# Optimization experiments

Measured on AMD Instinct MI355X. Metric: run time of the kernel, lower is better.

The kernel has to match this reference:

```python
import jax, jax.numpy as jnp
from jax import lax
import numpy as np

B, C, T = 8, 512, 2048
D = C // 2  # inter_channels
EPS = 1e-5


def setup_inputs() -> dict:
    key = jax.random.key(0)
    ks = jax.random.split(key, 16)
    inp = {}
    inp['x'] = jax.random.normal(ks[0], (B, C, T), dtype=jnp.float32)
    # temporal convs: Conv2d(1, C, kernel=(3, C), dilation=(i+1,1)), no bias, std=0.001
    inp['tc_w1'] = jax.random.normal(ks[1], (C, 1, 3, C), dtype=jnp.float32) * 0.001
    inp['tc_w2'] = jax.random.normal(ks[2], (C, 1, 3, C), dtype=jnp.float32) * 0.001
    # z: Conv1d(3C -> C, k=1)
    inp['z_w'] = jax.random.normal(ks[3], (C, 3 * C), dtype=jnp.float32) * (1.0 / np.sqrt(3 * C))
    inp['z_b'] = jax.random.normal(ks[4], (C,), dtype=jnp.float32) * 0.02
    # g / theta / phi: Conv1d(C -> D, k=1)
    s = 1.0 / np.sqrt(C)
    inp['g_w'] = jax.random.normal(ks[5], (D, C), dtype=jnp.float32) * s
    inp['g_b'] = jax.random.normal(ks[6], (D,), dtype=jnp.float32) * 0.02
    inp['th_w'] = jax.random.normal(ks[7], (D, C), dtype=jnp.float32) * s
    inp['th_b'] = jax.random.normal(ks[8], (D,), dtype=jnp.float32) * 0.02
    inp['ph_w'] = jax.random.normal(ks[9], (D, C), dtype=jnp.float32) * s
    inp['ph_b'] = jax.random.normal(ks[10], (D,), dtype=jnp.float32) * 0.02
    # W: Conv1d(D -> C, k=1) + BatchNorm1d(C) (eval-mode with trained params)
    inp['W_w'] = jax.random.normal(ks[11], (C, D), dtype=jnp.float32) * (1.0 / np.sqrt(D))
    inp['W_b'] = jax.random.normal(ks[12], (C,), dtype=jnp.float32) * 0.02
    inp['bn_g'] = jax.random.normal(ks[13], (C,), dtype=jnp.float32) * 0.1 + 1.0
    inp['bn_b'] = jax.random.normal(ks[14], (C,), dtype=jnp.float32) * 0.1
    inp['bn_mean'] = jax.random.normal(ks[15], (C,), dtype=jnp.float32) * 0.1
    inp['bn_var'] = jax.random.uniform(jax.random.fold_in(key, 99), (C,), dtype=jnp.float32) + 0.5
    return inp


def _pos_encoding(t, c):
    # standard sinusoidal PE, shape (t, c)
    pos = jnp.arange(t, dtype=jnp.float32)[:, None]
    div = jnp.exp(-jnp.log(jnp.float32(10000.0)) * (jnp.arange(0, c, 2, dtype=jnp.float32) / c))
    pe = jnp.zeros((t, c), dtype=jnp.float32)
    pe = pe.at[:, 0::2].set(jnp.sin(pos * div))
    pe = pe.at[:, 1::2].set(jnp.cos(pos * div))
    return pe


def _conv1x1(w, b, x):
    # w: (O, I), x: (b, I, T) -> (b, O, T)
    return jnp.einsum('oi,bit->bot', w, x) + b[None, :, None]


def _tconv(xt, w, d):
    # xt: (b, 1, T, C), w: (C_out, 1, 3, C), dilation d along T, padding (d, 0)
    out = lax.conv_general_dilated(
        xt, w, window_strides=(1, 1), padding=[(d, d), (0, 0)],
        rhs_dilation=(d, 1), dimension_numbers=('NCHW', 'OIHW', 'NCHW'))
    return out[..., 0]  # (b, C_out, T)


def reference(x, tc_w1, tc_w2, z_w, z_b, g_w, g_b, th_w, th_b, ph_w, ph_b,
              W_w, W_b, bn_g, bn_b, bn_mean, bn_var):
    b, c, t = x.shape
    # positional-encoding add: pos (b, T, C) -> permute -> (b, C, T)
    pe = _pos_encoding(t, c)           # (T, C)
    x = x + pe.T[None]                 # (b, C, T)
    # temporal dilated convs over (b, 1, T, C)
    xt = x.transpose(0, 2, 1)[:, None]  # (b, 1, T, C)
    temp = jnp.concatenate([_tconv(xt, tc_w1, 1), _tconv(xt, tc_w2, 2)], axis=1)  # (b, 2C, T)
    xcat = jnp.concatenate([x, temp], axis=1)   # (b, 3C, T)
    x2 = _conv1x1(z_w, z_b, xcat)               # (b, C, T)
    g_x = _conv1x1(g_w, g_b, x2).transpose(0, 2, 1)    # (b, T, D)
    theta_x = _conv1x1(th_w, th_b, x2).transpose(0, 2, 1)  # (b, T, D)
    phi_x = _conv1x1(ph_w, ph_b, x2)            # (b, D, T)
    f = jnp.einsum('btd,bds->bts', theta_x, phi_x)  # unscaled affinity (b, T, T)
    f_div_C = jax.nn.softmax(f, axis=-1)
    y = jnp.einsum('bts,bsd->btd', f_div_C, g_x)    # (b, T, D)
    y = y.transpose(0, 2, 1)                         # (b, D, T)
    wy = _conv1x1(W_w, W_b, y)                       # (b, C, T)
    # BatchNorm1d (eval mode)
    wy = (wy - bn_mean[None, :, None]) * (bn_g / jnp.sqrt(bn_var + EPS))[None, :, None] + bn_b[None, :, None]
    return wy + x2
```

## Files before the change

kernel.cpp:

```cpp
#include <hip/hip_runtime.h>
#include <stdint.h>

typedef _Float16 h8v __attribute__((ext_vector_type(8)));
typedef float f4v __attribute__((ext_vector_type(4)));

#define MFMA(a,b,c) __builtin_amdgcn_mfma_f32_16x16x32_f16((a),(b),(c),0,0,0)
#define NSPLIT 4

__device__ __forceinline__ _Float16 f2h(float f) { return (_Float16)f; }

__device__ __forceinline__ int swb(int row, int chunk) {
  return row * 64 + (((chunk) ^ ((row >> 1) & 3)) << 4);
}

__global__ __launch_bounds__(256) void k_pe_t(const float* __restrict__ x, _Float16* __restrict__ xpe) {
  __shared__ float tile[32][33];
  int b = blockIdx.z;
  int t0 = blockIdx.x * 32, c0 = blockIdx.y * 32;
  int tid = threadIdx.x;
  int col = tid & 31, rowq = tid >> 5;
#pragma unroll
  for (int i = 0; i < 4; ++i) {
    int c = c0 + rowq + i * 8;
    int t = t0 + col;
    int j2 = c & ~1;
    float dv = expf(-0.01798894603885192f * (float)j2);
    float ang = (float)t * dv;
    float pe = (c & 1) ? cosf(ang) : sinf(ang);
    tile[rowq + i * 8][col] = x[((size_t)b * 512 + c) * 2048 + t] + pe;
  }
  __syncthreads();
#pragma unroll
  for (int i = 0; i < 4; ++i) {
    int t = t0 + rowq + i * 8;
    int c = c0 + col;
    xpe[((size_t)b * 2048 + t) * 512 + c] = f2h(tile[col][rowq + i * 8]);
  }
}

__global__ __launch_bounds__(256) void k_cast(const float* __restrict__ a0, const float* __restrict__ a1,
                                              const float* __restrict__ a2, const float* __restrict__ a3,
                                              _Float16* __restrict__ o) {
  int w = blockIdx.y;
  const float* s = (w == 0) ? a0 : (w == 1) ? a1 : (w == 2) ? a2 : a3;
  int i = blockIdx.x * 256 + threadIdx.x;
  o[(size_t)w * 131072 + i] = f2h(s[i]);
}

__global__ __launch_bounds__(256) void k_castz(const float* __restrict__ zw, _Float16* __restrict__ zh) {
  int i = blockIdx.x * 256 + threadIdx.x;
  zh[i] = f2h(zw[i]);
}

__global__ __launch_bounds__(256) void k_wtrans(const float* __restrict__ w1, const float* __restrict__ w2,
                                                _Float16* __restrict__ wt) {
  int z = blockIdx.z;
  const float* src = (z < 3) ? w1 : w2;
  int k = (z < 3) ? z : z - 3;
  __shared__ _Float16 tile[64][65];
  int m0 = blockIdx.y * 64, c0 = blockIdx.x * 64;
  int tid = threadIdx.x;
  int tc = tid & 63, tm = tid >> 6;
#pragma unroll
  for (int i = 0; i < 16; ++i) {
    int m = m0 + tm + i * 4;
    tile[tm + i * 4][tc] = f2h(src[(size_t)m * 1536 + (size_t)k * 512 + c0 + tc]);
  }
  __syncthreads();
#pragma unroll
  for (int i = 0; i < 16; ++i) {
    int c = c0 + tm + i * 4;
    wt[((size_t)z * 512 + c) * 512 + m0 + tc] = tile[tc][tm + i * 4];
  }
}

__global__ __launch_bounds__(256) void k_merge(const _Float16* __restrict__ zh,
                                               const _Float16* __restrict__ wt,
                                               const float* __restrict__ zwf,
                                               _Float16* __restrict__ M) {
  int s = blockIdx.z;
  int wid = threadIdx.x >> 6, lane = threadIdx.x & 63;
  int o0 = blockIdx.y * 64 + (wid >> 1) * 32;
  int c0 = blockIdx.x * 64 + (wid & 1) * 32;
  int row16 = lane & 15, kg = lane >> 4, koff = kg * 8;
  f4v acc[2][2];
#pragma unroll
  for (int mi = 0; mi < 2; ++mi)
#pragma unroll
    for (int ni = 0; ni < 2; ++ni) acc[mi][ni] = (f4v){0.f, 0.f, 0.f, 0.f};

  int np = (s == 2) ? 2 : 1;
  for (int p = 0; p < np; ++p) {
    int seg, wi;
    if (s == 0)      { seg = 1024; wi = 3; }
    else if (s == 1) { seg = 512;  wi = 0; }
    else if (s == 3) { seg = 512;  wi = 2; }
    else if (s == 4) { seg = 1024; wi = 5; }
    else             { seg = (p == 0) ? 512 : 1024; wi = (p == 0) ? 1 : 4; }
    const _Float16* A = zh + seg;
    const _Float16* B = wt + (size_t)wi * 512 * 512;
    for (int k0 = 0; k0 < 512; k0 += 32) {
      h8v a[2], bv[2];
#pragma unroll
      for (int i = 0; i < 2; ++i)
        a[i] = *(const h8v*)(A + (size_t)(o0 + i * 16 + row16) * 1536 + k0 + koff);
#pragma unroll
      for (int i = 0; i < 2; ++i)
        bv[i] = *(const h8v*)(B + (size_t)(c0 + i * 16 + row16) * 512 + k0 + koff);
#pragma unroll
      for (int mi = 0; mi < 2; ++mi)
#pragma unroll
        for (int ni = 0; ni < 2; ++ni)
          acc[mi][ni] = MFMA(a[mi], bv[ni], acc[mi][ni]);
    }
  }
  _Float16* dst = M + (size_t)s * 512 * 512;
#pragma unroll
  for (int mi = 0; mi < 2; ++mi)
#pragma unroll
    for (int r = 0; r < 4; ++r) {
      int o = o0 + mi * 16 + kg * 4 + r;
#pragma unroll
      for (int ni = 0; ni < 2; ++ni) {
        int c = c0 + ni * 16 + row16;
        float v = acc[mi][ni][r];
        if (s == 2) v += zwf[(size_t)o * 1536 + c];
        dst[(size_t)o * 512 + c] = f2h(v);
      }
    }
}

__device__ __forceinline__ void gemm128_lds(const _Float16* __restrict__ L, int ldl,
                                            const _Float16* __restrict__ R, int ldr,
                                            int K, int tid, char* lsA, char* lsB,
                                            f4v acc[4][4]) {
  int wid = tid >> 6, lane = tid & 63;
  int wm = (wid >> 1) * 64, wn = (wid & 1) * 64;
  int row16 = lane & 15, kg = lane >> 4;
  int ar0 = tid >> 2, ar1 = (tid + 256) >> 2, ach = tid & 3;
  h8v pa0, pa1, pb0, pb1;

  pa0 = *(const h8v*)(L + (size_t)ar0 * ldl + ach * 8);
  pa1 = *(const h8v*)(L + (size_t)ar1 * ldl + ach * 8);
  pb0 = *(const h8v*)(R + (size_t)ar0 * ldr + ach * 8);
  pb1 = *(const h8v*)(R + (size_t)ar1 * ldr + ach * 8);
  *(h8v*)(lsA + swb(ar0, ach)) = pa0;
  *(h8v*)(lsA + swb(ar1, ach)) = pa1;
  *(h8v*)(lsB + swb(ar0, ach)) = pb0;
  *(h8v*)(lsB + swb(ar1, ach)) = pb1;
  __syncthreads();

  int nk = K >> 5;
  for (int kc = 0; kc < nk; ++kc) {
    char* ca = lsA + (kc & 1) * 8192;
    char* cb = lsB + (kc & 1) * 8192;
    bool pf = (kc < nk - 1);
    if (pf) {
      int k1 = (kc + 1) << 5;
      pa0 = *(const h8v*)(L + (size_t)ar0 * ldl + k1 + ach * 8);
      pa1 = *(const h8v*)(L + (size_t)ar1 * ldl + k1 + ach * 8);
      pb0 = *(const h8v*)(R + (size_t)ar0 * ldr + k1 + ach * 8);
      pb1 = *(const h8v*)(R + (size_t)ar1 * ldr + k1 + ach * 8);
    }
    h8v a[4], bv[4];
#pragma unroll
    for (int i = 0; i < 4; ++i)
      a[i] = *(const h8v*)(ca + swb(wm + i * 16 + row16, kg));
#pragma unroll
    for (int i = 0; i < 4; ++i)
      bv[i] = *(const h8v*)(cb + swb(wn + i * 16 + row16, kg));
#pragma unroll
    for (int mi = 0; mi < 4; ++mi)
#pragma unroll
      for (int ni = 0; ni < 4; ++ni)
        acc[mi][ni] = MFMA(a[mi], bv[ni], acc[mi][ni]);
    if (pf) {
      char* na = lsA + ((kc & 1) ^ 1) * 8192;
      char* nb = lsB + ((kc & 1) ^ 1) * 8192;
      *(h8v*)(na + swb(ar0, ach)) = pa0;
      *(h8v*)(na + swb(ar1, ach)) = pa1;
      *(h8v*)(nb + swb(ar0, ach)) = pb0;
      *(h8v*)(nb + swb(ar1, ach)) = pb1;
    }
    __syncthreads();
  }
}

__global__ __launch_bounds__(256, 2) void k_conv(const _Float16* __restrict__ Mh,
                                                 const _Float16* __restrict__ xpe,
                                                 const float* __restrict__ zb,
                                                 _Float16* __restrict__ x2ct,
                                                 _Float16* __restrict__ x2h) {
  int b = blockIdx.z;
  int o0 = blockIdx.y * 64, t0 = blockIdx.x * 128;
  int tid = threadIdx.x;
  int wid = tid >> 6, lane = tid & 63;
  int wm = (wid >> 1) * 32, wn = (wid & 1) * 64;
  int row16 = lane & 15, kg = lane >> 4;
  __shared__ __align__(16) char asm2[2][320 * 64];
  __shared__ __align__(16) char bsm[2][132 * 64];
  const _Float16* Xb = xpe + (size_t)b * 2048 * 512;
  const h8v zerov = {0, 0, 0, 0, 0, 0, 0, 0};

  f4v acc[2][4];
#pragma unroll
  for (int mi = 0; mi < 2; ++mi)
#pragma unroll
    for (int ni = 0; ni < 4; ++ni) acc[mi][ni] = (f4v){0.f, 0.f, 0.f, 0.f};

  int arow[5], asrow[5], aorow[5], achk = tid & 3;
#pragma unroll
  for (int j = 0; j < 5; ++j) {
    arow[j] = (tid + 256 * j) >> 2;
    asrow[j] = arow[j] >> 6;
    aorow[j] = arow[j] & 63;
  }
  int br0 = tid >> 2, br1 = (tid + 256) >> 2, br2 = (tid + 512) >> 2;
  int tg0 = t0 + br0 - 2, tg1 = t0 + br1 - 2, tg2 = t0 + br2 - 2;
  bool v0 = (tg0 >= 0 && tg0 < 2048);
  bool v1 = (tg1 >= 0 && tg1 < 2048);
  bool v2 = (tid < 16) && (tg2 >= 0 && tg2 < 2048);
  h8v sa[5], s0, s1, s2;

#pragma unroll
  for (int j = 0; j < 5; ++j)
    sa[j] = *(const h8v*)(Mh + (size_t)asrow[j] * 262144 + (size_t)(o0 + aorow[j]) * 512 + achk * 8);
  s0 = v0 ? *(const h8v*)(Xb + (size_t)tg0 * 512 + achk * 8) : zerov;
  s1 = v1 ? *(const h8v*)(Xb + (size_t)tg1 * 512 + achk * 8) : zerov;
  s2 = v2 ? *(const h8v*)(Xb + (size_t)tg2 * 512 + achk * 8) : zerov;
#pragma unroll
  for (int j = 0; j < 5; ++j) *(h8v*)(&asm2[0][swb(arow[j], achk)]) = sa[j];
  *(h8v*)(&bsm[0][swb(br0, achk)]) = s0;
  *(h8v*)(&bsm[0][swb(br1, achk)]) = s1;
  if (tid < 16) *(h8v*)(&bsm[0][swb(br2, achk)]) = s2;
  __syncthreads();

  for (int kc = 0; kc < 16; ++kc) {
    char* ca = asm2[kc & 1];
    char* cb = bsm[kc & 1];
    bool pf = (kc < 15);
    if (pf) {
      int k1 = (kc + 1) * 32;
#pragma unroll
      for (int j = 0; j < 5; ++j)
        sa[j] = *(const h8v*)(Mh + (size_t)asrow[j] * 262144 + (size_t)(o0 + aorow[j]) * 512 + k1 + achk * 8);
      s0 = v0 ? *(const h8v*)(Xb + (size_t)tg0 * 512 + k1 + achk * 8) : zerov;
      s1 = v1 ? *(const h8v*)(Xb + (size_t)tg1 * 512 + k1 + achk * 8) : zerov;
      s2 = v2 ? *(const h8v*)(Xb + (size_t)tg2 * 512 + k1 + achk * 8) : zerov;
    }
#pragma unroll
    for (int s = 0; s < 5; ++s) {
      h8v a[2];
#pragma unroll
      for (int i = 0; i < 2; ++i)
        a[i] = *(const h8v*)(ca + swb(s * 64 + wm + i * 16 + row16, kg));
#pragma unroll
      for (int ni = 0; ni < 4; ++ni) {
        int rr = wn + ni * 16 + row16 + s;
        h8v bv = *(const h8v*)(cb + swb(rr, kg));
#pragma unroll
        for (int mi = 0; mi < 2; ++mi)
          acc[mi][ni] = MFMA(a[mi], bv, acc[mi][ni]);
      }
    }
    if (pf) {
      char* na = asm2[(kc & 1) ^ 1];
      char* nb = bsm[(kc & 1) ^ 1];
#pragma unroll
      for (int j = 0; j < 5; ++j) *(h8v*)(&na[swb(arow[j], achk)]) = sa[j];
      *(h8v*)(&nb[swb(br0, achk)]) = s0;
      *(h8v*)(&nb[swb(br1, achk)]) = s1;
      if (tid < 16) *(h8v*)(&nb[swb(br2, achk)]) = s2;
    }
    __syncthreads();
  }

#pragma unroll
  for (int mi = 0; mi < 2; ++mi)
#pragma unroll
    for (int r = 0; r < 4; ++r) {
      int o = o0 + wm + mi * 16 + kg * 4 + r;
      float bias = zb[o];
#pragma unroll
      for (int ni = 0; ni < 4; ++ni) {
        int t = t0 + wn + ni * 16 + row16;
        float v = acc[mi][ni][r] + bias;
        x2ct[((size_t)b * 512 + o) * 2048 + t] = f2h(v);
        x2h[((size_t)b * 2048 + t) * 512 + o] = f2h(v);
      }
    }
}

__global__ __launch_bounds__(256, 3) void k_gtp(const _Float16* __restrict__ x2h,
                                                const _Float16* __restrict__ wth, const _Float16* __restrict__ wph,
                                                const _Float16* __restrict__ wg,
                                                const float* __restrict__ thb, const float* __restrict__ phb,
                                                const float* __restrict__ gb,
                                                _Float16* __restrict__ tht, _Float16* __restrict__ pht,
                                                _Float16* __restrict__ gv) {
  int b = blockIdx.z;
  int proj = blockIdx.y >> 1, dtile = blockIdx.y & 1;
  int tid = threadIdx.x;
  int wid = tid >> 6, lane = tid & 63;
  int wm = (wid >> 1) * 64, wn = (wid & 1) * 64;
  int row16 = lane & 15, kg = lane >> 4;
  __shared__ __align__(16) char lA[2][8192];
  __shared__ __align__(16) char lB[2][8192];
  const _Float16* X = x2h + (size_t)b * 2048 * 512;
  f4v acc[4][4];
#pragma unroll
  for (int mi = 0; mi < 4; ++mi)
#pragma unroll
    for (int ni = 0; ni < 4; ++ni) acc[mi][ni] = (f4v){0.f, 0.f, 0.f, 0.f};

  if (proj < 2) {
    const _Float16* W = (proj == 0) ? wth : wph;
    const float* bias = (proj == 0) ? thb : phb;
    _Float16* out = (proj == 0) ? tht : pht;
    int m0 = blockIdx.x * 128, n0 = dtile * 128;
    gemm128_lds(X + (size_t)m0 * 512, 512, W + (size_t)n0 * 512, 512, 512, tid, lA[0], lB[0], acc);
#pragma unroll
    for (int mi = 0; mi < 4; ++mi)
#pragma unroll
      for (int r = 0; r < 4; ++r) {
        int t = m0 + wm + mi * 16 + kg * 4 + r;
#pragma unroll
        for (int ni = 0; ni < 4; ++ni) {
          int d = n0 + wn + ni * 16 + row16;
          out[((size_t)b * 2048 + t) * 256 + d] = f2h(acc[mi][ni][r] + bias[d]);
        }
      }
  } else {
    int m0 = dtile * 128, n0 = blockIdx.x * 128;
    gemm128_lds(wg + (size_t)m0 * 512, 512, X + (size_t)n0 * 512, 512, 512, tid, lA[0], lB[0], acc);
#pragma unroll
    for (int mi = 0; mi < 4; ++mi)
#pragma unroll
      for (int r = 0; r < 4; ++r) {
        int d = m0 + wm + mi * 16 + kg * 4 + r;
        float bias = gb[d];
#pragma unroll
        for (int ni = 0; ni < 4; ++ni) {
          int t = n0 + wn + ni * 16 + row16;
          gv[((size_t)b * 256 + d) * 2048 + t] = f2h(acc[mi][ni][r] + bias);
        }
      }
  }
}

__global__ __launch_bounds__(512) void k_attn(const _Float16* __restrict__ tht,
                                              const _Float16* __restrict__ pht,
                                              const _Float16* __restrict__ gv,
                                              _Float16* __restrict__ yp,
                                              float* __restrict__ mlm, float* __restrict__ mll) {
  int b = blockIdx.z, sp = blockIdx.y;
  int tid = threadIdx.x;
  int wid = tid >> 6, lane = tid & 63;
  int q0 = blockIdx.x * 128 + wid * 16;
  int row16 = lane & 15, kg = lane >> 4, koff = kg * 8;
  int rswz = row16 & 7;

  __shared__ __align__(16) _Float16 kvbuf[32768];
  __shared__ __align__(16) _Float16 p_lds[8][1024];
  char* pw = (char*)&p_lds[wid][0];
  char* cb = (char*)&kvbuf[0];

  const _Float16* thb = tht + (size_t)b * 2048 * 256;
  const _Float16* phb = pht + (size_t)b * 2048 * 256;
  const _Float16* gvb = gv + (size_t)b * 256 * 2048;

  h8v qf[8];
#pragma unroll
  for (int ks = 0; ks < 8; ++ks)
    qf[ks] = *(const h8v*)(thb + (size_t)(q0 + row16) * 256 + ks * 32 + koff);

  float m_i[4], l_i[4];
#pragma unroll
  for (int r = 0; r < 4; ++r) { m_i[r] = -3e38f; l_i[r] = 0.f; }
  f4v yacc[16];
#pragma unroll
  for (int ni = 0; ni < 16; ++ni) yacc[ni] = (f4v){0.f, 0.f, 0.f, 0.f};

  {
    int k0 = sp * 512;
#pragma unroll
    for (int j = 0; j < 4; ++j) {
      int idx = tid + 512 * j;
      h8v kv = *(const h8v*)(phb + (size_t)(k0 + (idx >> 5)) * 256 + (idx & 31) * 8);
      h8v vv = *(const h8v*)(gvb + (size_t)(idx >> 3) * 2048 + k0 + (idx & 7) * 8);
      *(h8v*)(cb + (idx >> 5) * 512 + (((idx & 31) ^ ((idx >> 5) & 7)) << 4)) = kv;
      *(h8v*)(cb + 32768 + (idx >> 3) * 128 + (((idx & 7) ^ ((idx >> 3) & 7)) << 4)) = vv;
    }
  }
  __syncthreads();

  for (int t = 0; t < 8; ++t) {
    int k0 = sp * 512 + t * 64;

    h8v kreg[4], vreg[4];
    bool pf = (t < 7);
    if (pf) {
      int k1 = k0 + 64;
#pragma unroll
      for (int j = 0; j < 4; ++j) {
        int idx = tid + 512 * j;
        kreg[j] = *(const h8v*)(phb + (size_t)(k1 + (idx >> 5)) * 256 + (idx & 31) * 8);
        vreg[j] = *(const h8v*)(gvb + (size_t)(idx >> 3) * 2048 + k1 + (idx & 7) * 8);
      }
    }

    f4v sacc[4];
#pragma unroll
    for (int ni = 0; ni < 4; ++ni) sacc[ni] = (f4v){0.f, 0.f, 0.f, 0.f};
#pragma unroll
    for (int ks = 0; ks < 8; ++ks) {
#pragma unroll
      for (int ni = 0; ni < 4; ++ni) {
        int krow = ni * 16 + row16;
        h8v kf = *(const h8v*)(cb + krow * 512 + ((((ks << 2) | kg) ^ rswz) << 4));
        sacc[ni] = MFMA(qf[ks], kf, sacc[ni]);
      }
    }
    float al[4];
#pragma unroll
    for (int r = 0; r < 4; ++r) {
      float rm = fmaxf(fmaxf(sacc[0][r], sacc[1][r]), fmaxf(sacc[2][r], sacc[3][r]));
#pragma unroll
      for (int m = 1; m <= 8; m <<= 1) rm = fmaxf(rm, __shfl_xor(rm, m, 64));
      float mn = fmaxf(m_i[r], rm);
      al[r] = __expf(m_i[r] - mn);
      m_i[r] = mn;
      float rs = 0.f;
#pragma unroll
      for (int ni = 0; ni < 4; ++ni) {
        float p = __expf(sacc[ni][r] - mn);
        sacc[ni][r] = p;
        rs += p;
      }
#pragma unroll
      for (int m = 1; m <= 8; m <<= 1) rs += __shfl_xor(rs, m, 64);
      l_i[r] = l_i[r] * al[r] + rs;
    }
#pragma unroll
    for (int r = 0; r < 4; ++r) {
      int q = kg * 4 + r;
#pragma unroll
      for (int ni = 0; ni < 4; ++ni) {
        int sx = ni * 16 + row16;
        int byte = (q * 128 + sx * 2) ^ ((q & 7) << 4);
        *(_Float16*)(pw + byte) = f2h(sacc[ni][r]);
      }
    }
#pragma unroll
    for (int ni = 0; ni < 16; ++ni)
#pragma unroll
      for (int r = 0; r < 4; ++r) yacc[ni][r] *= al[r];
#pragma unroll
    for (int ks2 = 0; ks2 < 2; ++ks2) {
      int pbyte = (row16 * 128 + (ks2 * 32 + koff) * 2) ^ (rswz << 4);
      h8v pa = *(const h8v*)(pw + pbyte);
#pragma unroll
      for (int ni = 0; ni < 16; ++ni) {
        int d = ni * 16 + row16;
        h8v vb = *(const h8v*)(cb + 32768 + d * 128 + ((((ks2 << 2) | kg) ^ rswz) << 4));
        yacc[ni] = MFMA(pa, vb, yacc[ni]);
      }
    }
    if (pf) {
      __syncthreads();
#pragma unroll
      for (int j = 0; j < 4; ++j) {
        int idx = tid + 512 * j;
        *(h8v*)(cb + (idx >> 5) * 512 + (((idx & 31) ^ ((idx >> 5) & 7)) << 4)) = kreg[j];
        *(h8v*)(cb + 32768 + (idx >> 3) * 128 + (((idx & 7) ^ ((idx >> 3) & 7)) << 4)) = vreg[j];
      }
      __syncthreads();
    }
  }

  _Float16* yb = yp + (size_t)(sp * 8 + b) * 2048 * 256;
  float* mm = mlm + (size_t)(sp * 8 + b) * 2048;
  float* ml = mll + (size_t)(sp * 8 + b) * 2048;
#pragma unroll
  for (int r = 0; r < 4; ++r) {
    int q = q0 + kg * 4 + r;
#pragma unroll
    for (int ni = 0; ni < 16; ++ni)
      yb[(size_t)q * 256 + ni * 16 + row16] = f2h(yacc[ni][r]);
    if (row16 == 0) { mm[q] = m_i[r]; ml[q] = l_i[r]; }
  }
}

__global__ __launch_bounds__(256) void k_comb(const _Float16* __restrict__ yp,
                                              const float* __restrict__ mlm, const float* __restrict__ mll,
                                              _Float16* __restrict__ yv) {
  int b = blockIdx.y;
  int q = blockIdx.x * 32 + (threadIdx.x >> 3);
  int d0 = (threadIdx.x & 7) * 32;
  float ms[NSPLIT], w[NSPLIT];
  float M = -3e38f;
#pragma unroll
  for (int s = 0; s < NSPLIT; ++s) {
    ms[s] = mlm[(size_t)(s * 8 + b) * 2048 + q];
    M = fmaxf(M, ms[s]);
  }
  float L = 0.f;
#pragma unroll
  for (int s = 0; s < NSPLIT; ++s) {
    w[s] = __expf(ms[s] - M);
    L += w[s] * mll[(size_t)(s * 8 + b) * 2048 + q];
  }
  float inv = 1.f / L;
#pragma unroll
  for (int s = 0; s < NSPLIT; ++s) w[s] *= inv;
  _Float16* out = yv + ((size_t)b * 2048 + q) * 256 + d0;
#pragma unroll
  for (int c = 0; c < 4; ++c) {
    float o[8];
#pragma unroll
    for (int j = 0; j < 8; ++j) o[j] = 0.f;
#pragma unroll
    for (int s = 0; s < NSPLIT; ++s) {
      h8v v = *(const h8v*)(yp + ((size_t)(s * 8 + b) * 2048 + q) * 256 + d0 + c * 8);
#pragma unroll
      for (int j = 0; j < 8; ++j) o[j] += w[s] * (float)v[j];
    }
    h8v ov;
#pragma unroll
    for (int j = 0; j < 8; ++j) ov[j] = f2h(o[j]);
    *(h8v*)(out + c * 8) = ov;
  }
}

__global__ __launch_bounds__(256, 3) void k_final(const _Float16* __restrict__ Wh,
                                                  const _Float16* __restrict__ yv,
                                                  const float* __restrict__ Wb,
                                                  const float* __restrict__ bng, const float* __restrict__ bnb,
                                                  const float* __restrict__ bnm, const float* __restrict__ bnv,
                                                  const _Float16* __restrict__ x2ct, float* __restrict__ out) {
  int b = blockIdx.z;
  int o0 = blockIdx.y * 128, t0 = blockIdx.x * 128;
  int tid = threadIdx.x;
  int wid = tid >> 6, lane = tid & 63;
  int wm = (wid >> 1) * 64, wn = (wid & 1) * 64;
  int row16 = lane & 15, kg = lane >> 4;
  __shared__ __align__(16) char lA[2][8192];
  __shared__ __align__(16) char lB[2][8192];
  f4v acc[4][4];
#pragma unroll
  for (int mi = 0; mi < 4; ++mi)
#pragma unroll
    for (int ni = 0; ni < 4; ++ni) acc[mi][ni] = (f4v){0.f, 0.f, 0.f, 0.f};
  gemm128_lds(Wh + (size_t)o0 * 256, 256,
              yv + (size_t)b * 2048 * 256 + (size_t)t0 * 256, 256, 256, tid, lA[0], lB[0], acc);
#pragma unroll
  for (int mi = 0; mi < 4; ++mi)
#pragma unroll
    for (int r = 0; r < 4; ++r) {
      int o = o0 + wm + mi * 16 + kg * 4 + r;
      float sc = bng[o] * rsqrtf(bnv[o] + 1e-5f);
      float add = (Wb[o] - bnm[o]) * sc + bnb[o];
#pragma unroll
      for (int ni = 0; ni < 4; ++ni) {
        int t = t0 + wn + ni * 16 + row16;
        size_t idx = ((size_t)b * 512 + o) * 2048 + t;
        out[idx] = acc[mi][ni][r] * sc + add + (float)x2ct[idx];
      }
    }
}

extern "C" void kernel_launch(void* const* d_in, const int* in_sizes, int n_in,
                              void* d_out, int out_size, void* d_ws, size_t ws_size,
                              hipStream_t stream) {
  const float* x    = (const float*)d_in[0];
  const float* tcw1 = (const float*)d_in[1];
  const float* tcw2 = (const float*)d_in[2];
  const float* zw   = (const float*)d_in[3];
  const float* zb   = (const float*)d_in[4];
  const float* gw   = (const float*)d_in[5];
  const float* gb   = (const float*)d_in[6];
  const float* thw  = (const float*)d_in[7];
  const float* thb  = (const float*)d_in[8];
  const float* phw  = (const float*)d_in[9];
  const float* phb  = (const float*)d_in[10];
  const float* Ww   = (const float*)d_in[11];
  const float* Wb   = (const float*)d_in[12];
  const float* bng  = (const float*)d_in[13];
  const float* bnb  = (const float*)d_in[14];
  const float* bnm  = (const float*)d_in[15];
  const float* bnv  = (const float*)d_in[16];

  char* Wp = (char*)d_ws;
  _Float16* xpe = (_Float16*)(Wp);
  _Float16* Mh  = (_Float16*)(Wp + 16777216);
  _Float16* x2h = (_Float16*)(Wp + 19398656);
  _Float16* x2c = (_Float16*)(Wp + 36175872);
  _Float16* tht = (_Float16*)(Wp + 69730304);
  _Float16* pht = (_Float16*)(Wp + 78118912);
  _Float16* gv  = (_Float16*)(Wp + 86507520);
  _Float16* yv  = (_Float16*)(Wp + 94896128);
  _Float16* wc  = (_Float16*)(Wp + 103284736);
  _Float16* wth = wc, *wph = wc + 131072, *wg = wc + 262144, *wW = wc + 393216;
  _Float16* zh  = (_Float16*)(Wp + 36175872);
  _Float16* wt  = (_Float16*)(Wp + 36175872 + 1572864);
  _Float16* yp  = (_Float16*)(Wp);
  float*    mlm = (float*)   (Wp + 33554432);
  float*    mll = (float*)   (Wp + 33816576);

  k_cast  <<<dim3(512, 4), 256, 0, stream>>>(thw, phw, gw, Ww, wc);
  k_castz <<<3072, 256, 0, stream>>>(zw, zh);
  k_wtrans<<<dim3(8, 8, 6), 256, 0, stream>>>(tcw1, tcw2, wt);
  k_merge <<<dim3(8, 8, 5), 256, 0, stream>>>(zh, wt, zw, Mh);
  k_pe_t  <<<dim3(64, 16, 8), 256, 0, stream>>>(x, xpe);
  k_conv  <<<dim3(16, 8, 8), 256, 0, stream>>>(Mh, xpe, zb, x2c, x2h);
  k_gtp   <<<dim3(16, 6, 8), 256, 0, stream>>>(x2h, wth, wph, wg, thb, phb, gb, tht, pht, gv);
  k_attn  <<<dim3(16, NSPLIT, 8), 512, 0, stream>>>(tht, pht, gv, yp, mlm, mll);
  k_comb  <<<dim3(64, 8), 256, 0, stream>>>(yp, mlm, mll, yv);
  k_final <<<dim3(16, 4, 8), 256, 0, stream>>>(wW, yv, Wb, bng, bnb, bnm, bnv, x2c, (float*)d_out);
}
```

Baseline: 224.3 us.

## Halve attention KV split, fuse split-combine into final GEMM, lazy softmax rescale

Attention now splits the keys two ways instead of four, and each block runs 16 tiles instead of 8. The separate combine kernel is removed: the final W-projection GEMM reads both partial outputs, merges them with weights derived from the max and sum, and writes the result into shared memory while loading its B operand. Online softmax now rescales the accumulator only when some row max grows by more than 8, which skips the per-tile multiply of the large y accumulator. This trades away attention parallelism (a smaller grid of 256 blocks) and lets the unnormalized exponentials reach up to e^8, a risk to fp16 precision.

```diff
diff --git a/kernel.cpp b/kernel.cpp
--- a/kernel.cpp
+++ b/kernel.cpp
@@ -5,7 +5,7 @@
 typedef float f4v __attribute__((ext_vector_type(4)));
 
 #define MFMA(a,b,c) __builtin_amdgcn_mfma_f32_16x16x32_f16((a),(b),(c),0,0,0)
-#define NSPLIT 4
+#define NSPLIT 2
 
 __device__ __forceinline__ _Float16 f2h(float f) { return (_Float16)f; }
 
@@ -382,7 +382,7 @@
   for (int ni = 0; ni < 16; ++ni) yacc[ni] = (f4v){0.f, 0.f, 0.f, 0.f};
 
   {
-    int k0 = sp * 512;
+    int k0 = sp * 1024;
 #pragma unroll
     for (int j = 0; j < 4; ++j) {
       int idx = tid + 512 * j;
@@ -394,11 +394,11 @@
   }
   __syncthreads();
 
-  for (int t = 0; t < 8; ++t) {
-    int k0 = sp * 512 + t * 64;
+  for (int t = 0; t < 16; ++t) {
+    int k0 = sp * 1024 + t * 64;
 
     h8v kreg[4], vreg[4];
-    bool pf = (t < 7);
+    bool pf = (t < 15);
     if (pf) {
       int k1 = k0 + 64;
 #pragma unroll
@@ -421,19 +421,35 @@
         sacc[ni] = MFMA(qf[ks], kf, sacc[ni]);
       }
     }
-    float al[4];
+    float al[4] = {1.f, 1.f, 1.f, 1.f};
+    float rmv[4];
+    float nd = 0.f;
 #pragma unroll
     for (int r = 0; r < 4; ++r) {
       float rm = fmaxf(fmaxf(sacc[0][r], sacc[1][r]), fmaxf(sacc[2][r], sacc[3][r]));
 #pragma unroll
       for (int m = 1; m <= 8; m <<= 1) rm = fmaxf(rm, __shfl_xor(rm, m, 64));
-      float mn = fmaxf(m_i[r], rm);
-      al[r] = __expf(m_i[r] - mn);
-      m_i[r] = mn;
+      rmv[r] = rm;
+      if (rm > m_i[r] + 8.f) nd = 1.f;
+    }
+    if (__any(nd != 0.f)) {
+#pragma unroll
+      for (int r = 0; r < 4; ++r) {
+        float mn = fmaxf(m_i[r], rmv[r]);
+        al[r] = __expf(m_i[r] - mn);
+        m_i[r] = mn;
+      }
+#pragma unroll
+      for (int ni = 0; ni < 16; ++ni)
+#pragma unroll
+        for (int r = 0; r < 4; ++r) yacc[ni][r] *= al[r];
+    }
+#pragma unroll
+    for (int r = 0; r < 4; ++r) {
       float rs = 0.f;
 #pragma unroll
       for (int ni = 0; ni < 4; ++ni) {
-        float p = __expf(sacc[ni][r] - mn);
+        float p = __expf(sacc[ni][r] - m_i[r]);
         sacc[ni][r] = p;
         rs += p;
       }
@@ -452,10 +468,6 @@
       }
     }
 #pragma unroll
-    for (int ni = 0; ni < 16; ++ni)
-#pragma unroll
-      for (int r = 0; r < 4; ++r) yacc[ni][r] *= al[r];
-#pragma unroll
     for (int ks2 = 0; ks2 < 2; ++ks2) {
       int pbyte = (row16 * 128 + (ks2 * 32 + koff) * 2) ^ (rswz << 4);
       h8v pa = *(const h8v*)(pw + pbyte);
@@ -491,49 +503,9 @@
   }
 }
 
-__global__ __launch_bounds__(256) void k_comb(const _Float16* __restrict__ yp,
-                                              const float* __restrict__ mlm, const float* __restrict__ mll,
-                                              _Float16* __restrict__ yv) {
-  int b = blockIdx.y;
-  int q = blockIdx.x * 32 + (threadIdx.x >> 3);
-  int d0 = (threadIdx.x & 7) * 32;
-  float ms[NSPLIT], w[NSPLIT];
-  float M = -3e38f;
-#pragma unroll
-  for (int s = 0; s < NSPLIT; ++s) {
-    ms[s] = mlm[(size_t)(s * 8 + b) * 2048 + q];
-    M = fmaxf(M, ms[s]);
-  }
-  float L = 0.f;
-#pragma unroll
-  for (int s = 0; s < NSPLIT; ++s) {
-    w[s] = __expf(ms[s] - M);
-    L += w[s] * mll[(size_t)(s * 8 + b) * 2048 + q];
-  }
-  float inv = 1.f / L;
-#pragma unroll
-  for (int s = 0; s < NSPLIT; ++s) w[s] *= inv;
-  _Float16* out = yv + ((size_t)b * 2048 + q) * 256 + d0;
-#pragma unroll
-  for (int c = 0; c < 4; ++c) {
-    float o[8];
-#pragma unroll
-    for (int j = 0; j < 8; ++j) o[j] = 0.f;
-#pragma unroll
-    for (int s = 0; s < NSPLIT; ++s) {
-      h8v v = *(const h8v*)(yp + ((size_t)(s * 8 + b) * 2048 + q) * 256 + d0 + c * 8);
-#pragma unroll
-      for (int j = 0; j < 8; ++j) o[j] += w[s] * (float)v[j];
-    }
-    h8v ov;
-#pragma unroll
-    for (int j = 0; j < 8; ++j) ov[j] = f2h(o[j]);
-    *(h8v*)(out + c * 8) = ov;
-  }
-}
-
 __global__ __launch_bounds__(256, 3) void k_final(const _Float16* __restrict__ Wh,
-                                                  const _Float16* __restrict__ yv,
+                                                  const _Float16* __restrict__ yp,
+                                                  const float* __restrict__ mlm, const float* __restrict__ mll,
                                                   const float* __restrict__ Wb,
                                                   const float* __restrict__ bng, const float* __restrict__ bnb,
                                                   const float* __restrict__ bnm, const float* __restrict__ bnv,
@@ -551,8 +523,81 @@
   for (int mi = 0; mi < 4; ++mi)
 #pragma unroll
     for (int ni = 0; ni < 4; ++ni) acc[mi][ni] = (f4v){0.f, 0.f, 0.f, 0.f};
-  gemm128_lds(Wh + (size_t)o0 * 256, 256,
-              yv + (size_t)b * 2048 * 256 + (size_t)t0 * 256, 256, 256, tid, lA[0], lB[0], acc);
+
+  const _Float16* L = Wh + (size_t)o0 * 256;
+  const _Float16* Y0 = yp + ((size_t)b * 2048 + t0) * 256;
+  const _Float16* Y1 = yp + ((size_t)(8 + b) * 2048 + t0) * 256;
+  int ar0 = tid >> 2, ar1 = ar0 + 64, ach = tid & 3;
+
+  float w0a, w1a, w0b, w1b;
+  {
+    int qa = t0 + ar0, qb = t0 + ar1;
+    float mA0 = mlm[(size_t)b * 2048 + qa], mA1 = mlm[(size_t)(8 + b) * 2048 + qa];
+    float Ma = fmaxf(mA0, mA1);
+    float e0 = __expf(mA0 - Ma), e1 = __expf(mA1 - Ma);
+    float La = e0 * mll[(size_t)b * 2048 + qa] + e1 * mll[(size_t)(8 + b) * 2048 + qa];
+    float ia = 1.f / La;
+    w0a = e0 * ia; w1a = e1 * ia;
+    float mB0 = mlm[(size_t)b * 2048 + qb], mB1 = mlm[(size_t)(8 + b) * 2048 + qb];
+    float Mb = fmaxf(mB0, mB1);
+    float f0 = __expf(mB0 - Mb), f1 = __expf(mB1 - Mb);
+    float Lb = f0 * mll[(size_t)b * 2048 + qb] + f1 * mll[(size_t)(8 + b) * 2048 + qb];
+    float ib = 1.f / Lb;
+    w0b = f0 * ib; w1b = f1 * ib;
+  }
+
+  h8v pa0, pa1, pb0, pb1;
+  auto comb = [&](const _Float16* y0, const _Float16* y1, float w0, float w1) -> h8v {
+    h8v u = *(const h8v*)y0, v = *(const h8v*)y1, o;
+#pragma unroll
+    for (int j = 0; j < 8; ++j) o[j] = f2h(w0 * (float)u[j] + w1 * (float)v[j]);
+    return o;
+  };
+
+  pa0 = *(const h8v*)(L + (size_t)ar0 * 256 + ach * 8);
+  pa1 = *(const h8v*)(L + (size_t)ar1 * 256 + ach * 8);
+  pb0 = comb(Y0 + (size_t)ar0 * 256 + ach * 8, Y1 + (size_t)ar0 * 256 + ach * 8, w0a, w1a);
+  pb1 = comb(Y0 + (size_t)ar1 * 256 + ach * 8, Y1 + (size_t)ar1 * 256 + ach * 8, w0b, w1b);
+  *(h8v*)(lA[0] + swb(ar0, ach)) = pa0;
+  *(h8v*)(lA[0] + swb(ar1, ach)) = pa1;
+  *(h8v*)(lB[0] + swb(ar0, ach)) = pb0;
+  *(h8v*)(lB[0] + swb(ar1, ach)) = pb1;
+  __syncthreads();
+
+  for (int kc = 0; kc < 8; ++kc) {
+    char* ca = lA[kc & 1];
+    char* cbp = lB[kc & 1];
+    bool pf = (kc < 7);
+    if (pf) {
+      int k1 = (kc + 1) << 5;
+      pa0 = *(const h8v*)(L + (size_t)ar0 * 256 + k1 + ach * 8);
+      pa1 = *(const h8v*)(L + (size_t)ar1 * 256 + k1 + ach * 8);
+      pb0 = comb(Y0 + (size_t)ar0 * 256 + k1 + ach * 8, Y1 + (size_t)ar0 * 256 + k1 + ach * 8, w0a, w1a);
+      pb1 = comb(Y0 + (size_t)ar1 * 256 + k1 + ach * 8, Y1 + (size_t)ar1 * 256 + k1 + ach * 8, w0b, w1b);
+    }
+    h8v a[4], bv[4];
+#pragma unroll
+    for (int i = 0; i < 4; ++i)
+      a[i] = *(const h8v*)(ca + swb(wm + i * 16 + row16, kg));
+#pragma unroll
+    for (int i = 0; i < 4; ++i)
+      bv[i] = *(const h8v*)(cbp + swb(wn + i * 16 + row16, kg));
+#pragma unroll
+    for (int mi = 0; mi < 4; ++mi)
+#pragma unroll
+      for (int ni = 0; ni < 4; ++ni)
+        acc[mi][ni] = MFMA(a[mi], bv[ni], acc[mi][ni]);
+    if (pf) {
+      char* na = lA[(kc & 1) ^ 1];
+      char* nb = lB[(kc & 1) ^ 1];
+      *(h8v*)(na + swb(ar0, ach)) = pa0;
+      *(h8v*)(na + swb(ar1, ach)) = pa1;
+      *(h8v*)(nb + swb(ar0, ach)) = pb0;
+      *(h8v*)(nb + swb(ar1, ach)) = pb1;
+    }
+    __syncthreads();
+  }
+
 #pragma unroll
   for (int mi = 0; mi < 4; ++mi)
 #pragma unroll
@@ -598,14 +643,13 @@
   _Float16* tht = (_Float16*)(Wp + 69730304);
   _Float16* pht = (_Float16*)(Wp + 78118912);
   _Float16* gv  = (_Float16*)(Wp + 86507520);
-  _Float16* yv  = (_Float16*)(Wp + 94896128);
   _Float16* wc  = (_Float16*)(Wp + 103284736);
   _Float16* wth = wc, *wph = wc + 131072, *wg = wc + 262144, *wW = wc + 393216;
   _Float16* zh  = (_Float16*)(Wp + 36175872);
   _Float16* wt  = (_Float16*)(Wp + 36175872 + 1572864);
   _Float16* yp  = (_Float16*)(Wp);
-  float*    mlm = (float*)   (Wp + 33554432);
-  float*    mll = (float*)   (Wp + 33816576);
+  float*    mlm = (float*)   (Wp + 16777216);
+  float*    mll = (float*)   (Wp + 16908288);
 
   k_cast  <<<dim3(512, 4), 256, 0, stream>>>(thw, phw, gw, Ww, wc);
   k_castz <<<3072, 256, 0, stream>>>(zw, zh);
@@ -615,6 +659,5 @@
   k_conv  <<<dim3(16, 8, 8), 256, 0, stream>>>(Mh, xpe, zb, x2c, x2h);
   k_gtp   <<<dim3(16, 6, 8), 256, 0, stream>>>(x2h, wth, wph, wg, thb, phb, gb, tht, pht, gv);
   k_attn  <<<dim3(16, NSPLIT, 8), 512, 0, stream>>>(tht, pht, gv, yp, mlm, mll);
-  k_comb  <<<dim3(64, 8), 256, 0, stream>>>(yp, mlm, mll, yv);
-  k_final <<<dim3(16, 4, 8), 256, 0, stream>>>(wW, yv, Wb, bng, bnb, bnm, bnv, x2c, (float*)d_out);
-}
+  k_final <<<dim3(16, 4, 8), 256, 0, stream>>>(wW, yp, mlm, mll, Wb, bng, bnb, bnm, bnv, x2c, (float*)d_out);
+}
```

After: 214.3 us. 4.5% less time.
